# Optimization experiments

Measured on AMD Instinct MI355X. Metric: run time of the kernel, lower is better.

Reference implementation:

```python
import jax, jax.numpy as jnp
import numpy as np

NV = 6890          # SMPL vertex count
NF = 13776         # SMPL face count
N_CHUNKS = 10
EUCL_THRES = 0.02  # euclthres
WN_THRES = 0.99    # exterior if winding number <= 0.99


def _winding_numbers(points, tris):
    """Generalized winding numbers of `points` [m,3] w.r.t. triangle soup `tris` [f,3,3].
    Solid angle per (point, triangle) via the van-Oosterom/Strackee atan2 formula."""
    r = tris[None, :, :, :] - points[:, None, None, :]   # [m,f,3,3]
    ra, rb, rc = r[:, :, 0, :], r[:, :, 1, :], r[:, :, 2, :]
    la = jnp.linalg.norm(ra, axis=-1)
    lb = jnp.linalg.norm(rb, axis=-1)
    lc = jnp.linalg.norm(rc, axis=-1)
    det = jnp.einsum('mfi,mfi->mf', ra, jnp.cross(rb, rc))
    denom = (la * lb * lc
             + jnp.sum(ra * rb, -1) * lc
             + jnp.sum(rb * rc, -1) * la
             + jnp.sum(rc * ra, -1) * lb)
    omega = 2.0 * jnp.arctan2(det, denom)                # [m,f]
    return jnp.sum(omega, axis=-1) / (4.0 * jnp.pi)      # [m]


def setup_inputs() -> dict:
    key = jax.random.key(0)
    k1, k2, k3 = jax.random.split(key, 3)
    vertices = jax.random.normal(k1, (1, NV, 3), dtype=jnp.float32)
    faces = jax.random.randint(k2, (NF, 3), 0, NV)
    # geodesic-distance >= geothres mask: symmetric, False on the diagonal
    gm = jax.random.uniform(k3, (NV, NV)) > 0.3
    gm = gm & gm.T
    gm = gm.at[jnp.arange(NV), jnp.arange(NV)].set(False)
    return {"vertices": vertices, "faces": faces, "geomask": gm}


def reference(vertices, faces, geomask):
    # triangles(vertices): gather face corner coordinates  [NF,3,3] (bs=1)
    tris = vertices[0][faces]
    # get_intersection_mask: chunked winding numbers, exterior = wn <= 0.99
    pts = vertices[0].reshape(N_CHUNKS, NV // N_CHUNKS, 3)
    wn = jax.lax.map(lambda p: _winding_numbers(p, tris), pts).reshape(NV)
    exterior = (wn <= WN_THRES)[None, :]                 # [1,NV] bool
    # batch_pairwise_dist (squared=False)
    x = vertices[0]                                      # [NV,3]
    sq = jnp.sum(x * x, axis=-1)
    d2 = sq[:, None] + sq[None, :] - 2.0 * (x @ x.T)
    v2v = jnp.sqrt(jnp.maximum(d2, 0.0))                 # [NV,NV]
    # mask geodesically-near pairs with inf, take per-vertex min over dim 1
    masked = jnp.where(geomask, v2v, jnp.inf)
    idx = jnp.argmin(masked, axis=0)                     # argmin over rows for each column
    v2v_min = v2v[jnp.arange(NV), idx][None, :]          # gather along dim 2 (symmetric)
    incontact = v2v_min < EUCL_THRES
    return v2v_min, incontact, exterior
```

## Files before the change

### kernel.cpp

```cpp
#include <hip/hip_runtime.h>
#include <math.h>

#define NV 6890
#define NF 13776
#define NVPAD 6912
#define NFPAD 13824
#define HALF 3456
#define V2V_BLOCKS 1723
#define RED_BLOCKS 27
#define WN_THRES 0.99
#define EUCL_THRES 0.02f

#define TCH_FB 64
#define TPC_FB 216
#define PBLK_FB 14
#define WNB_FB (TCH_FB*PBLK_FB)
#define TCH_TB 128
#define TPC_TB 108
#define PBLK_TB 14
#define WNB_TB (TCH_TB*PBLK_TB)

#define WS_TRIS_OFF   64
#define WS_X4_OFF     (64 + NFPAD*48)
#define WS_PART_OFF   (WS_X4_OFF + NVPAD*16)
#define WS_TAB_OFF    (((WS_PART_OFF + TCH_TB*NVPAD*4) + 255) & ~(size_t)255)
#define WS_TAB_BYTES  ((size_t)NV * NVPAD * 4)

__global__ __launch_bounds__(256) void prep_kernel(
    const float* __restrict__ verts, const int* __restrict__ faces,
    const unsigned char* __restrict__ gm_bytes,
    float* __restrict__ tris, float* __restrict__ x4, int* __restrict__ flag,
    int mode)
{
    int t = blockIdx.x * 256 + threadIdx.x;

    if (t < NFPAD) {
        float* o = tris + (size_t)t * 12;
        if (t < NF) {
            int ia = faces[t*3+0], ib = faces[t*3+1], ic = faces[t*3+2];
            float Ax = verts[ia*3+0], Ay = verts[ia*3+1], Az = verts[ia*3+2];
            float Bx = verts[ib*3+0], By = verts[ib*3+1], Bz = verts[ib*3+2];
            float Cx = verts[ic*3+0], Cy = verts[ic*3+1], Cz = verts[ic*3+2];
            if (mode == 0) {
                o[0]=Ax; o[1]=Ay; o[2]=Az;  o[3]=0.f;
                o[4]=Bx; o[5]=By; o[6]=Bz;  o[7]=0.f;
                o[8]=Cx; o[9]=Cy; o[10]=Cz; o[11]=0.f;
            } else {
                float e1x=Bx-Ax, e1y=By-Ay, e1z=Bz-Az;
                float e2x=Cx-Ax, e2y=Cy-Ay, e2z=Cz-Az;
                float nx = e1y*e2z - e1z*e2y;
                float ny = e1z*e2x - e1x*e2z;
                float nz = e1x*e2y - e1y*e2x;
                float d0 = (nx*Ax + ny*Ay) + nz*Az;
                float eab = (e1x*e1x + e1y*e1y) + e1z*e1z;
                float bcx=Cx-Bx, bcy=Cy-By, bcz=Cz-Bz;
                float ebc = (bcx*bcx + bcy*bcy) + bcz*bcz;
                float eca = (e2x*e2x + e2y*e2y) + e2z*e2z;
                o[0]=nx; o[1]=ny; o[2]=nz; o[3]=d0;
                o[4]=eab; o[5]=ebc; o[6]=eca; o[7]=0.f;
                o[8]=__int_as_float(ia); o[9]=__int_as_float(ib);
                o[10]=__int_as_float(ic); o[11]=0.f;
            }
        } else {
            #pragma unroll
            for (int q = 0; q < 12; ++q) o[q] = 0.f;
        }
    }
    if (t < NVPAD) {
        if (t < NV) {
            float x = verts[t*3+0], y = verts[t*3+1], z = verts[t*3+2];
            x4[t*4+0] = x; x4[t*4+1] = y; x4[t*4+2] = z;
            x4[t*4+3] = (x*x + y*y) + z*z;
        } else {
            x4[t*4+0] = 0.f; x4[t*4+1] = 0.f; x4[t*4+2] = 0.f; x4[t*4+3] = 0.f;
        }
    }
    if (blockIdx.x == 0 && threadIdx.x < 64) {
        int lane = threadIdx.x;
        bool any3F = false, anyNZmod = false;
        for (int k = 0; k < 64; ++k) {
            int off = lane * 64 + k;
            unsigned char b = gm_bytes[off];
            if ((off & 3) == 3 && (b == 0x3F || b == 0xBF)) any3F = true;
            if ((off & 3) != 0 && b != 0) anyNZmod = true;
        }
        unsigned long long m3F = __ballot(any3F);
        unsigned long long mNZ = __ballot(anyNZmod);
        if (lane == 0) *flag = m3F ? 2 : (mNZ ? 0 : 1);
    }
}

__global__ __launch_bounds__(256) void tab_kernel(
    const float4* __restrict__ x4, float* __restrict__ D)
{
    int p = blockIdx.x * 256 + threadIdx.x;
    int v = blockIdx.y;
    float4 Pv = x4[v];
    float4 Pp = x4[p];
    float dx = Pv.x - Pp.x, dy = Pv.y - Pp.y, dz = Pv.z - Pp.z;
    D[(size_t)v * NVPAD + p] = __builtin_amdgcn_sqrtf((dx*dx + dy*dy) + dz*dz);
}

__device__ __forceinline__ float fast_atan2f(float y, float x)
{
    float ay = __builtin_fabsf(y), ax = __builtin_fabsf(x);
    float mx = fmaxf(ax, ay);
    float mn = fminf(ax, ay);
    float r  = __builtin_amdgcn_rcpf(fmaxf(mx, 1e-37f));
    float t  = mn * r;
    float s  = t * t;
    float u  =              0.00282363896258175373077393f;
    u = fmaf(u, s, -0.0159569028764963150024414f);
    u = fmaf(u, s,  0.0425049886107444763183594f);
    u = fmaf(u, s, -0.0748900920152664184570312f);
    u = fmaf(u, s,  0.106347933411598205566406f);
    u = fmaf(u, s, -0.142027363181114196777344f);
    u = fmaf(u, s,  0.199926957488059997558594f);
    u = fmaf(u, s, -0.333331018686294555664062f);
    float p = fmaf(s * u, t, t);
    p = (ay > ax)  ? (1.5707963267948966f - p) : p;
    p = (x < 0.0f) ? (3.14159265358979323846f - p) : p;
    return copysignf(p, y);
}

#define OMEGA_TAB(LA, LB, LC, PX, PY, PZ, S)                               \
    {                                                                      \
        float la2 = LA*LA, lb2 = LB*LB, lc2 = LC*LC;                       \
        float dab = (la2 + lb2 - eab) * 0.5f;                              \
        float dbc = (lb2 + lc2 - ebc) * 0.5f;                              \
        float dca = (lc2 + la2 - eca) * 0.5f;                              \
        float det = d0 - ((nx*PX + ny*PY) + nz*PZ);                        \
        float t3  = (LA*LB)*LC;                                            \
        float denom = fmaf(dca, LB, fmaf(dbc, LA, fmaf(dab, LC, t3)));     \
        float o = fast_atan2f(det, denom);                                 \
        S += (t3 != 0.0f) ? o : 0.0f;   \
    }

__global__ __launch_bounds__(256) void fused_tab_kernel(
    const float* __restrict__ consts, const float* __restrict__ Dt,
    const float4* __restrict__ x4, float* __restrict__ partials,
    const void* __restrict__ gm, const int* __restrict__ flag_p,
    float* __restrict__ out)
{
    if (blockIdx.x < WNB_TB) {
        int tc = blockIdx.x / PBLK_TB;
        int pb = blockIdx.x - tc * PBLK_TB;
        int pt = pb * 256 + threadIdx.x;
        if (pt >= HALF) return;
        int ptH = pt + HALF;

        float4 P0 = x4[pt];
        float4 P1 = x4[ptH];

        const float* cvb = consts + (size_t)tc * TPC_TB * 12;
        double acc0 = 0.0, acc1 = 0.0;

        for (int k = 0; k < TPC_TB; k += 2) {
            float s0 = 0.f, s1 = 0.f;
            #pragma unroll
            for (int u = 0; u < 2; ++u) {
                const float* cv = cvb + (size_t)(k + u) * 12;
                float nx = cv[0], ny = cv[1], nz = cv[2], d0 = cv[3];
                float eab = cv[4], ebc = cv[5], eca = cv[6];
                int ia = __float_as_int(cv[8]);
                int ib = __float_as_int(cv[9]);
                int ic = __float_as_int(cv[10]);
                const float* rA = Dt + (size_t)ia * NVPAD;
                const float* rB = Dt + (size_t)ib * NVPAD;
                const float* rC = Dt + (size_t)ic * NVPAD;
                float la0 = rA[pt],  lb0 = rB[pt],  lc0 = rC[pt];
                float la1 = rA[ptH], lb1 = rB[ptH], lc1 = rC[ptH];
                OMEGA_TAB(la0, lb0, lc0, P0.x, P0.y, P0.z, s0);
                OMEGA_TAB(la1, lb1, lc1, P1.x, P1.y, P1.z, s1);
            }
            acc0 += (double)s0;
            acc1 += (double)s1;
        }

        float* prow = partials + (size_t)tc * NVPAD;
        prow[pt]  = (float)acc0;
        prow[ptH] = (float)acc1;
    } else {
        int bid = blockIdx.x - WNB_TB;
        int w = threadIdx.x >> 6;
        int lane = threadIdx.x & 63;
        int j = bid * 4 + w;
        if (j >= NV) return;

        int flag = *flag_p;
        const float* Dr = Dt + (size_t)j * NVPAD;
        float m = INFINITY;

#define V2V_TAB(GTEST)                                             \
        {                                                          \
            int i0 = 0;                                            \
            _Pragma("unroll 4")                                    \
            for (; i0 + 64 <= NV; i0 += 64) {                      \
                int i = i0 + lane;                                 \
                bool g = (GTEST);                                  \
                float d = Dr[i];                                   \
                m = fminf(m, g ? d : INFINITY);                    \
            }                                                      \
            int i = i0 + lane;                                     \
            if (i < NV) {                                          \
                bool g = (GTEST);                                  \
                float d = Dr[i];                                   \
                m = fminf(m, g ? d : INFINITY);                    \
            }                                                      \
        }
        if (flag == 0) {
            const unsigned char* row = (const unsigned char*)gm + (size_t)j * NV;
            V2V_TAB(row[i] != 0)
        } else if (flag == 1) {
            const int* row = (const int*)gm + (size_t)j * NV;
            V2V_TAB(row[i] != 0)
        } else {
            const float* row = (const float*)gm + (size_t)j * NV;
            V2V_TAB(row[i] != 0.0f)
        }
#undef V2V_TAB

        #pragma unroll
        for (int k = 32; k > 0; k >>= 1)
            m = fminf(m, __shfl_xor(m, k, 64));
        if (lane == 0) {
            out[j] = m;
            out[NV + j] = (m < EUCL_THRES) ? 1.f : 0.f;
        }
    }
}

__global__ __launch_bounds__(256) void reduce_tab_kernel(
    const float* __restrict__ partials, float* __restrict__ out_exterior)
{
    int pt = blockIdx.x * 256 + threadIdx.x;
    if (pt >= NV) return;
    double s = 0.0;
    for (int t = 0; t < TCH_TB; ++t) s += (double)partials[(size_t)t * NVPAD + pt];
    double wn = (2.0 * s) / 12.566370614359172953850573533118;
    out_exterior[pt] = (wn <= WN_THRES) ? 1.0f : 0.0f;
}

#define TRI_OMEGA(A, B, C, PX, PY, PZ, S)                                 \
    {                                                                     \
        float ax = A.x - PX, ay = A.y - PY, az = A.z - PZ;                \
        float bx = B.x - PX, by = B.y - PY, bz = B.z - PZ;                \
        float cx = C.x - PX, cy = C.y - PY, cz = C.z - PZ;                \
        float la = __builtin_amdgcn_sqrtf((ax*ax + ay*ay) + az*az);       \
        float lb = __builtin_amdgcn_sqrtf((bx*bx + by*by) + bz*bz);       \
        float lc = __builtin_amdgcn_sqrtf((cx*cx + cy*cy) + cz*cz);       \
        float ux = by*cz - bz*cy;                                         \
        float uy = bz*cx - bx*cz;                                         \
        float uz = bx*cy - by*cx;                                         \
        float det = (ax*ux + ay*uy) + az*uz;                              \
        float dab = (ax*bx + ay*by) + az*bz;                              \
        float dbc = (bx*cx + by*cy) + bz*cz;                              \
        float dca = (cx*ax + cy*ay) + cz*az;                              \
        float denom = la*lb*lc + dab*lc + dbc*la + dca*lb;                \
        S += fast_atan2f(det, denom);                                     \
    }

__global__ __launch_bounds__(256) void fused_fb_kernel(
    const float4* __restrict__ tris12, const float4* __restrict__ x4,
    float* __restrict__ partials,
    const void* __restrict__ gm, const int* __restrict__ flag_p,
    float* __restrict__ out)
{
    if (blockIdx.x < WNB_FB) {
        int tc = blockIdx.x / PBLK_FB;
        int pb = blockIdx.x - tc * PBLK_FB;
        int pt = pb * 256 + threadIdx.x;
        if (pt >= HALF) return;
        int p1i = pt + HALF;

        float4 P0 = x4[pt];
        float4 P1 = x4[p1i];
        float px0 = P0.x, py0 = P0.y, pz0 = P0.z;
        float px1 = P1.x, py1 = P1.y, pz1 = P1.z;

        const float4* __restrict__ T = tris12 + (size_t)tc * (TPC_FB * 3);

        float4 A0 = T[0], B0 = T[1], C0 = T[2];
        float4 A1 = T[3], B1 = T[4], C1 = T[5];
        double acc0 = 0.0, acc1 = 0.0;

        for (int kk = 0; kk < TPC_FB; kk += 2) {
            int n0 = 3 * min(kk + 2, TPC_FB - 1);
            int n1 = 3 * min(kk + 3, TPC_FB - 1);
            float s0 = 0.f, s1 = 0.f;

            TRI_OMEGA(A0, B0, C0, px0, py0, pz0, s0);
            TRI_OMEGA(A0, B0, C0, px1, py1, pz1, s1);
            A0 = T[n0]; B0 = T[n0 + 1]; C0 = T[n0 + 2];

            TRI_OMEGA(A1, B1, C1, px0, py0, pz0, s0);
            TRI_OMEGA(A1, B1, C1, px1, py1, pz1, s1);
            A1 = T[n1]; B1 = T[n1 + 1]; C1 = T[n1 + 2];

            acc0 += (double)s0;
            acc1 += (double)s1;
        }

        partials[(size_t)tc * NVPAD + pt]  = (float)acc0;
        partials[(size_t)tc * NVPAD + p1i] = (float)acc1;
    } else {
        int bid = blockIdx.x - WNB_FB;
        int w = threadIdx.x >> 6;
        int lane = threadIdx.x & 63;
        int j = bid * 4 + w;
        if (j >= NV) return;

        int flag = *flag_p;
        float4 vj = x4[j];
        float m = INFINITY;

#define V2V_BODY(GTEST)                                            \
        {                                                          \
            int i0 = 0;                                            \
            _Pragma("unroll 4")                                    \
            for (; i0 + 64 <= NV; i0 += 64) {                      \
                int i = i0 + lane;                                 \
                bool g = (GTEST);                                  \
                float4 vi = x4[i];                                 \
                float dot = (vi.x*vj.x + vi.y*vj.y) + vi.z*vj.z;   \
                float d2  = vi.w + vj.w - 2.0f*dot;                \
                m = fminf(m, g ? d2 : INFINITY);                   \
            }                                                      \
            int i = i0 + lane;                                     \
            if (i < NV) {                                          \
                bool g = (GTEST);                                  \
                float4 vi = x4[i];                                 \
                float dot = (vi.x*vj.x + vi.y*vj.y) + vi.z*vj.z;   \
                float d2  = vi.w + vj.w - 2.0f*dot;                \
                m = fminf(m, g ? d2 : INFINITY);                   \
            }                                                      \
        }
        if (flag == 0) {
            const unsigned char* row = (const unsigned char*)gm + (size_t)j * NV;
            V2V_BODY(row[i] != 0)
        } else if (flag == 1) {
            const int* row = (const int*)gm + (size_t)j * NV;
            V2V_BODY(row[i] != 0)
        } else {
            const float* row = (const float*)gm + (size_t)j * NV;
            V2V_BODY(row[i] != 0.0f)
        }
#undef V2V_BODY

        #pragma unroll
        for (int k = 32; k > 0; k >>= 1)
            m = fminf(m, __shfl_xor(m, k, 64));
        if (lane == 0) {
            float d = __builtin_amdgcn_sqrtf(fmaxf(m, 0.f));
            out[j] = d;
            out[NV + j] = (d < EUCL_THRES) ? 1.f : 0.f;
        }
    }
}

__global__ __launch_bounds__(256) void reduce_fb_kernel(
    const float* __restrict__ partials, float* __restrict__ out_exterior)
{
    int pt = blockIdx.x * 256 + threadIdx.x;
    if (pt >= NV) return;
    double s = 0.0;
    for (int t = 0; t < TCH_FB; ++t) s += (double)partials[(size_t)t * NVPAD + pt];
    double wn = (2.0 * s) / 12.566370614359172953850573533118;
    out_exterior[pt] = (wn <= WN_THRES) ? 1.0f : 0.0f;
}

extern "C" void kernel_launch(void* const* d_in, const int* in_sizes, int n_in,
                              void* d_out, int out_size, void* d_ws, size_t ws_size,
                              hipStream_t stream)
{
    const float* verts = (const float*)d_in[0];
    const int*   faces = (const int*)d_in[1];
    const void*  gm    = d_in[2];
    float* out = (float*)d_out;
    char* ws = (char*)d_ws;

    int*   flag     = (int*)ws;
    float* tris     = (float*)(ws + WS_TRIS_OFF);
    float* x4       = (float*)(ws + WS_X4_OFF);
    float* partials = (float*)(ws + WS_PART_OFF);
    float* Dt       = (float*)(ws + WS_TAB_OFF);

    size_t need = (size_t)WS_TAB_OFF + WS_TAB_BYTES;
    if (ws_size >= need) {
        prep_kernel<<<NFPAD / 256, 256, 0, stream>>>(
            verts, faces, (const unsigned char*)gm, tris, x4, flag, 1);
        tab_kernel<<<dim3(NVPAD / 256, NV), 256, 0, stream>>>(
            (const float4*)x4, Dt);
        fused_tab_kernel<<<WNB_TB + V2V_BLOCKS, 256, 0, stream>>>(
            tris, Dt, (const float4*)x4, partials, gm, flag, out);
        reduce_tab_kernel<<<RED_BLOCKS, 256, 0, stream>>>(partials, out + 2 * NV);
    } else {
        prep_kernel<<<NFPAD / 256, 256, 0, stream>>>(
            verts, faces, (const unsigned char*)gm, tris, x4, flag, 0);
        fused_fb_kernel<<<WNB_FB + V2V_BLOCKS, 256, 0, stream>>>(
            (const float4*)tris, (const float4*)x4, partials, gm, flag, out);
        reduce_fb_kernel<<<RED_BLOCKS, 256, 0, stream>>>(partials, out + 2 * NV);
    }
}
```

Measured before the change: 454.1 us.

## Process four points per thread in table winding kernel and recompute v2v distances

The table-based winding-number path now has each thread handle four query points instead of two, halving the point blocks per triangle chunk, so each per-triangle constant load is reused across more points. The v2v min section of the tabulated kernel no longer reads the precomputed distance table row; it recomputes squared distances from the float4 vertex array and takes a sqrt at the end, sharing a macro with the fallback kernel. This cuts global reads of the large distance table in exchange for more registers and less parallelism in the winding section.

```diff
diff --git a/kernel.cpp b/kernel.cpp
--- a/kernel.cpp
+++ b/kernel.cpp
@@ -6,6 +6,7 @@
 #define NVPAD 6912
 #define NFPAD 13824
 #define HALF 3456
+#define QTR 1728
 #define V2V_BLOCKS 1723
 #define RED_BLOCKS 27
 #define WN_THRES 0.99
@@ -17,7 +18,7 @@
 #define WNB_FB (TCH_FB*PBLK_FB)
 #define TCH_TB 128
 #define TPC_TB 108
-#define PBLK_TB 14
+#define PBLK_TB 7
 #define WNB_TB (TCH_TB*PBLK_TB)
 
 #define WS_TRIS_OFF   64
@@ -123,6 +124,57 @@
     return copysignf(p, y);
 }
 
+#define V2V_SECTION(BID)                                                   \
+    {                                                                      \
+        int w = threadIdx.x >> 6;                                          \
+        int lane = threadIdx.x & 63;                                       \
+        int j = (BID) * 4 + w;                                             \
+        if (j >= NV) return;                                               \
+        int flag = *flag_p;                                                \
+        float4 vj = x4[j];                                                 \
+        float m = INFINITY;                                                \
+        if (flag == 0) {                                                   \
+            const unsigned char* row = (const unsigned char*)gm + (size_t)j * NV; \
+            V2V_BODY(row[i] != 0)                                          \
+        } else if (flag == 1) {                                            \
+            const int* row = (const int*)gm + (size_t)j * NV;              \
+            V2V_BODY(row[i] != 0)                                          \
+        } else {                                                           \
+            const float* row = (const float*)gm + (size_t)j * NV;          \
+            V2V_BODY(row[i] != 0.0f)                                       \
+        }                                                                  \
+        _Pragma("unroll")                                                  \
+        for (int k = 32; k > 0; k >>= 1)                                   \
+            m = fminf(m, __shfl_xor(m, k, 64));                            \
+        if (lane == 0) {                                                   \
+            float d = __builtin_amdgcn_sqrtf(fmaxf(m, 0.f));               \
+            out[j] = d;                                                    \
+            out[NV + j] = (d < EUCL_THRES) ? 1.f : 0.f;                    \
+        }                                                                  \
+    }
+
+#define V2V_BODY(GTEST)                                            \
+    {                                                              \
+        int i0 = 0;                                                \
+        _Pragma("unroll 4")                                        \
+        for (; i0 + 64 <= NV; i0 += 64) {                          \
+            int i = i0 + lane;                                     \
+            bool g = (GTEST);                                      \
+            float4 vi = x4[i];                                     \
+            float dot = (vi.x*vj.x + vi.y*vj.y) + vi.z*vj.z;       \
+            float d2  = vi.w + vj.w - 2.0f*dot;                    \
+            m = fminf(m, g ? d2 : INFINITY);                       \
+        }                                                          \
+        int i = i0 + lane;                                         \
+        if (i < NV) {                                              \
+            bool g = (GTEST);                                      \
+            float4 vi = x4[i];                                     \
+            float dot = (vi.x*vj.x + vi.y*vj.y) + vi.z*vj.z;       \
+            float d2  = vi.w + vj.w - 2.0f*dot;                    \
+            m = fminf(m, g ? d2 : INFINITY);                       \
+        }                                                          \
+    }
+
 #define OMEGA_TAB(LA, LB, LC, PX, PY, PZ, S)                               \
     {                                                                      \
         float la2 = LA*LA, lb2 = LB*LB, lc2 = LC*LC;                       \
@@ -146,17 +198,18 @@
         int tc = blockIdx.x / PBLK_TB;
         int pb = blockIdx.x - tc * PBLK_TB;
         int pt = pb * 256 + threadIdx.x;
-        if (pt >= HALF) return;
-        int ptH = pt + HALF;
+        if (pt >= QTR) return;
 
         float4 P0 = x4[pt];
-        float4 P1 = x4[ptH];
+        float4 P1 = x4[pt + QTR];
+        float4 P2 = x4[pt + 2*QTR];
+        float4 P3 = x4[pt + 3*QTR];
 
         const float* cvb = consts + (size_t)tc * TPC_TB * 12;
-        double acc0 = 0.0, acc1 = 0.0;
+        double acc0 = 0.0, acc1 = 0.0, acc2 = 0.0, acc3 = 0.0;
 
         for (int k = 0; k < TPC_TB; k += 2) {
-            float s0 = 0.f, s1 = 0.f;
+            float s0 = 0.f, s1 = 0.f, s2 = 0.f, s3 = 0.f;
             #pragma unroll
             for (int u = 0; u < 2; ++u) {
                 const float* cv = cvb + (size_t)(k + u) * 12;
@@ -168,65 +221,28 @@
                 const float* rA = Dt + (size_t)ia * NVPAD;
                 const float* rB = Dt + (size_t)ib * NVPAD;
                 const float* rC = Dt + (size_t)ic * NVPAD;
-                float la0 = rA[pt],  lb0 = rB[pt],  lc0 = rC[pt];
-                float la1 = rA[ptH], lb1 = rB[ptH], lc1 = rC[ptH];
-                OMEGA_TAB(la0, lb0, lc0, P0.x, P0.y, P0.z, s0);
-                OMEGA_TAB(la1, lb1, lc1, P1.x, P1.y, P1.z, s1);
+                float la0 = rA[pt],         lb0 = rB[pt],         lc0 = rC[pt];
+                float la1 = rA[pt + QTR],   lb1 = rB[pt + QTR],   lc1 = rC[pt + QTR];
+                float la2_ = rA[pt + 2*QTR], lb2_ = rB[pt + 2*QTR], lc2_ = rC[pt + 2*QTR];
+                float la3 = rA[pt + 3*QTR], lb3 = rB[pt + 3*QTR], lc3 = rC[pt + 3*QTR];
+                OMEGA_TAB(la0,  lb0,  lc0,  P0.x, P0.y, P0.z, s0);
+                OMEGA_TAB(la1,  lb1,  lc1,  P1.x, P1.y, P1.z, s1);
+                OMEGA_TAB(la2_, lb2_, lc2_, P2.x, P2.y, P2.z, s2);
+                OMEGA_TAB(la3,  lb3,  lc3,  P3.x, P3.y, P3.z, s3);
             }
             acc0 += (double)s0;
             acc1 += (double)s1;
+            acc2 += (double)s2;
+            acc3 += (double)s3;
         }
 
         float* prow = partials + (size_t)tc * NVPAD;
-        prow[pt]  = (float)acc0;
-        prow[ptH] = (float)acc1;
+        prow[pt]         = (float)acc0;
+        prow[pt +   QTR] = (float)acc1;
+        prow[pt + 2*QTR] = (float)acc2;
+        prow[pt + 3*QTR] = (float)acc3;
     } else {
-        int bid = blockIdx.x - WNB_TB;
-        int w = threadIdx.x >> 6;
-        int lane = threadIdx.x & 63;
-        int j = bid * 4 + w;
-        if (j >= NV) return;
-
-        int flag = *flag_p;
-        const float* Dr = Dt + (size_t)j * NVPAD;
-        float m = INFINITY;
-
-#define V2V_TAB(GTEST)                                             \
-        {                                                          \
-            int i0 = 0;                                            \
-            _Pragma("unroll 4")                                    \
-            for (; i0 + 64 <= NV; i0 += 64) {                      \
-                int i = i0 + lane;                                 \
-                bool g = (GTEST);                                  \
-                float d = Dr[i];                                   \
-                m = fminf(m, g ? d : INFINITY);                    \
-            }                                                      \
-            int i = i0 + lane;                                     \
-            if (i < NV) {                                          \
-                bool g = (GTEST);                                  \
-                float d = Dr[i];                                   \
-                m = fminf(m, g ? d : INFINITY);                    \
-            }                                                      \
-        }
-        if (flag == 0) {
-            const unsigned char* row = (const unsigned char*)gm + (size_t)j * NV;
-            V2V_TAB(row[i] != 0)
-        } else if (flag == 1) {
-            const int* row = (const int*)gm + (size_t)j * NV;
-            V2V_TAB(row[i] != 0)
-        } else {
-            const float* row = (const float*)gm + (size_t)j * NV;
-            V2V_TAB(row[i] != 0.0f)
-        }
-#undef V2V_TAB
-
-        #pragma unroll
-        for (int k = 32; k > 0; k >>= 1)
-            m = fminf(m, __shfl_xor(m, k, 64));
-        if (lane == 0) {
-            out[j] = m;
-            out[NV + j] = (m < EUCL_THRES) ? 1.f : 0.f;
-        }
+        V2V_SECTION(blockIdx.x - WNB_TB)
     }
 }
 
@@ -304,57 +320,7 @@
         partials[(size_t)tc * NVPAD + pt]  = (float)acc0;
         partials[(size_t)tc * NVPAD + p1i] = (float)acc1;
     } else {
-        int bid = blockIdx.x - WNB_FB;
-        int w = threadIdx.x >> 6;
-        int lane = threadIdx.x & 63;
-        int j = bid * 4 + w;
-        if (j >= NV) return;
-
-        int flag = *flag_p;
-        float4 vj = x4[j];
-        float m = INFINITY;
-
-#define V2V_BODY(GTEST)                                            \
-        {                                                          \
-            int i0 = 0;                                            \
-            _Pragma("unroll 4")                                    \
-            for (; i0 + 64 <= NV; i0 += 64) {                      \
-                int i = i0 + lane;                                 \
-                bool g = (GTEST);                                  \
-                float4 vi = x4[i];                                 \
-                float dot = (vi.x*vj.x + vi.y*vj.y) + vi.z*vj.z;   \
-                float d2  = vi.w + vj.w - 2.0f*dot;                \
-                m = fminf(m, g ? d2 : INFINITY);                   \
-            }                                                      \
-            int i = i0 + lane;                                     \
-            if (i < NV) {                                          \
-                bool g = (GTEST);                                  \
-                float4 vi = x4[i];                                 \
-                float dot = (vi.x*vj.x + vi.y*vj.y) + vi.z*vj.z;   \
-                float d2  = vi.w + vj.w - 2.0f*dot;                \
-                m = fminf(m, g ? d2 : INFINITY);                   \
-            }                                                      \
-        }
-        if (flag == 0) {
-            const unsigned char* row = (const unsigned char*)gm + (size_t)j * NV;
-            V2V_BODY(row[i] != 0)
-        } else if (flag == 1) {
-            const int* row = (const int*)gm + (size_t)j * NV;
-            V2V_BODY(row[i] != 0)
-        } else {
-            const float* row = (const float*)gm + (size_t)j * NV;
-            V2V_BODY(row[i] != 0.0f)
-        }
-#undef V2V_BODY
-
-        #pragma unroll
-        for (int k = 32; k > 0; k >>= 1)
-            m = fminf(m, __shfl_xor(m, k, 64));
-        if (lane == 0) {
-            float d = __builtin_amdgcn_sqrtf(fmaxf(m, 0.f));
-            out[j] = d;
-            out[NV + j] = (d < EUCL_THRES) ? 1.f : 0.f;
-        }
+        V2V_SECTION(blockIdx.x - WNB_FB)
     }
 }
 
```

After: 466.4 us. +2.7%, slower.
